# Kernel optimization log

Hardware: AMD Instinct MI355X
Metric: run time of the kernel (lower is better)

The kernel has to match this reference:

```python
import jax, jax.numpy as jnp
import numpy as np

N_NODES = 50000
LN_EPS = 1e-5


def setup_inputs() -> dict:
    key = jax.random.key(0)
    ks = jax.random.split(key, 8)
    d = 128
    E = 800000
    x = jax.random.normal(ks[0], (N_NODES, d), dtype=jnp.float32)
    edge_index = jax.random.randint(ks[1], (2, E), 0, N_NODES, dtype=jnp.int64)
    edge_weight = jax.random.uniform(ks[2], (E,), dtype=jnp.float32)
    s = 1.0 / np.sqrt(d)
    W1 = jax.random.normal(ks[3], (d, d), dtype=jnp.float32) * s
    W2 = jax.random.normal(ks[4], (d, d), dtype=jnp.float32) * s
    return {
        'x': x, 'edge_index': edge_index, 'edge_weight': edge_weight,
        'W1': W1, 'b1': jnp.zeros((d,), jnp.float32),
        'W2': W2, 'b2': jnp.zeros((d,), jnp.float32),
        'g1': jnp.ones((d,), jnp.float32), 'be1': jnp.zeros((d,), jnp.float32),
        'g2': jnp.ones((d,), jnp.float32), 'be2': jnp.zeros((d,), jnp.float32),
    }


def _layer_norm(h, gamma, beta):
    mu = jnp.mean(h, axis=-1, keepdims=True)
    var = jnp.mean(jnp.square(h - mu), axis=-1, keepdims=True)
    return (h - mu) * jax.lax.rsqrt(var + LN_EPS) * gamma + beta


def _gcn_layer(h, W, b, src, dst, ew):
    # GCNConv(add_self_loops=False, normalize=False): linear then edge scatter-add
    h = h @ W                                    # [N, d]
    msg = h[src] * ew[:, None]                   # [E, d] gather + weight
    agg = jax.ops.segment_sum(msg, dst, num_segments=N_NODES)  # scatter-add at target
    return agg + b


def reference(x, edge_index, edge_weight, W1, b1, W2, b2, g1, be1, g2, be2):
    src, dst = edge_index[0], edge_index[1]  # PyG: messages flow source -> target
    h = _gcn_layer(x, W1, b1, src, dst, edge_weight)
    h = jax.nn.relu(_layer_norm(h, g1, be1))  # dropout = identity (eval)
    h = _gcn_layer(h, W2, b2, src, dst, edge_weight)
    h = jax.nn.relu(_layer_norm(h, g2, be2))
    return h
```

## Files before the change

### kernel.cpp

```cpp
#include <hip/hip_runtime.h>
#include <hip/hip_fp16.h>
#include <stdint.h>

#define LN_EPS 1e-5f
#define G1 256
#define P1CAP 4096
#define P3CAP 6144
#define CAPB 6144

typedef __attribute__((ext_vector_type(8))) short s16x8;
typedef __attribute__((ext_vector_type(4))) float f32x4;

__device__ __forceinline__ float b2f(unsigned short u) {
    union { unsigned int i; float f; } v; v.i = ((unsigned int)u) << 16; return v.f;
}
__device__ __forceinline__ unsigned short f2b(float f) {
    union { float f; unsigned int i; } v; v.f = f;
    unsigned int u = v.i;
    return (unsigned short)((u + 0x7fffu + ((u >> 16) & 1u)) >> 16);
}
__device__ __forceinline__ unsigned int pk2(float a, float b) {
    return (unsigned int)f2b(a) | ((unsigned int)f2b(b) << 16);
}
__device__ __forceinline__ __half2 u2h2(unsigned int u) {
    union { unsigned int i; __half2 h; } v; v.i = u; return v.h;
}

__device__ __forceinline__ float rdf(const void* p, int i, int f32flag) {
    return f32flag ? ((const float*)p)[i] : b2f(((const unsigned short*)p)[i]);
}

__global__ void k_prep(const void* W1, const void* W2,
                       const void* b1, const void* b2,
                       const void* g1, const void* g2,
                       const void* be1, const void* be2,
                       unsigned short* __restrict__ Wt1, unsigned short* __restrict__ Wt2,
                       float* __restrict__ sm, const int* __restrict__ flags) {
    int t = threadIdx.x;
    int f = flags[0];
    int i = blockIdx.x * 256 + t;
    int k = i >> 7, j = i & 127;
    Wt1[j * 128 + k] = f2b(rdf(W1, i, f));
    Wt2[j * 128 + k] = f2b(rdf(W2, i, f));
    if (blockIdx.x == 0 && t < 128) {
        sm[t]       = rdf(b1, t, f);
        sm[128 + t] = rdf(b2, t, f);
        sm[256 + t] = rdf(g1, t, f);
        sm[384 + t] = rdf(g2, t, f);
        sm[512 + t] = rdf(be1, t, f);
        sm[640 + t] = rdf(be2, t, f);
    }
}

__global__ __launch_bounds__(256) void k_p1(const unsigned short* __restrict__ xu,
                                            const int* __restrict__ ei, const void* __restrict__ ew,
                                            int E, int B, int chunk,
                                            unsigned int* __restrict__ gA,
                                            unsigned char* __restrict__ g8,
                                            int* __restrict__ cnt2d, int* __restrict__ lofs2d,
                                            int* __restrict__ flags) {
    __shared__ int hist[256], cur[256], tmp[256];
    __shared__ unsigned int bin32[P1CAP];
    __shared__ unsigned char bin8[P1CAP];
    int t = threadIdx.x, g = blockIdx.x;
    if (t < 2) hist[t] = 0;
    __syncthreads();
    int c1 = 0;
    for (int i = t; i < 2048; i += 256)
        if (fabsf(b2f(xu[i])) > 1e6f) ++c1;
    if (c1) atomicAdd(&hist[0], c1);
    int mn = (E < 1024) ? E : 1024;
    int z = 0;
    for (int i = t; i < mn; i += 256)
        if (ei[2 * i + 1] == 0) ++z;
    if (z) atomicAdd(&hist[1], z);
    __syncthreads();
    int f32f = (hist[0] > 32) ? 1 : 0;
    int f64  = (hist[1] > (mn >> 1)) ? 1 : 0;
    if (g == 0 && t == 0) { flags[0] = f32f; flags[1] = f64; }
    __syncthreads();
    int base = g * chunk;
    int cnt = E - base; if (cnt > chunk) cnt = chunk; if (cnt < 0) cnt = 0;
    hist[t] = 0;
    __syncthreads();
    for (int i = t; i < cnt; i += 256) {
        int e = base + i;
        int d = f64 ? ei[2 * E + 2 * e] : ei[E + e];
        atomicAdd(&hist[d >> 8], 1);
    }
    __syncthreads();
    int v = hist[t];
    tmp[t] = v;
    __syncthreads();
    for (int d = 1; d < 256; d <<= 1) {
        int x = (t >= d) ? tmp[t - d] : 0;
        __syncthreads();
        tmp[t] += x;
        __syncthreads();
    }
    int excl = tmp[t] - v;
    cur[t] = excl;
    if (t < B) { cnt2d[t * G1 + g] = v; lofs2d[t * G1 + g] = excl; }
    __syncthreads();
    for (int i = t; i < cnt; i += 256) {
        int e = base + i;
        int d, sN;
        if (f64) { d = ei[2 * E + 2 * e]; sN = ei[2 * e]; }
        else     { d = ei[E + e];         sN = ei[e]; }
        float w = f32f ? ((const float*)ew)[e] : b2f(((const unsigned short*)ew)[e]);
        __half wh = __float2half(w);
        int p = atomicAdd(&cur[d >> 8], 1);
        bin32[p] = (unsigned int)(sN & 0xffff) | ((unsigned int)__half_as_ushort(wh) << 16);
        bin8[p]  = (unsigned char)(d & 255);
    }
    __syncthreads();
    for (int j = t; j < cnt; j += 256) {
        gA[base + j] = bin32[j];
        g8[base + j] = bin8[j];
    }
}

__global__ __launch_bounds__(256) void k_p3(const unsigned int* __restrict__ gA,
                                            const unsigned char* __restrict__ g8,
                                            const int* __restrict__ cnt2d,
                                            const int* __restrict__ lofs2d,
                                            unsigned int* __restrict__ edata,
                                            uint2* __restrict__ nfo,
                                            int N, int B, int chunk) {
    __shared__ unsigned int raw[P3CAP];
    __shared__ unsigned int srt[CAPB];
    __shared__ unsigned char r8[P3CAP];
    __shared__ int h[256], tmp[256];
    __shared__ int s_cnt;
    int b = blockIdx.x, t = threadIdx.x;
    int segc = cnt2d[b * G1 + t];
    int sbase = t * chunk + lofs2d[b * G1 + t];
    int v = segc;
    tmp[t] = v;
    __syncthreads();
    for (int d = 1; d < 256; d <<= 1) {
        int x = (t >= d) ? tmp[t - d] : 0;
        __syncthreads();
        tmp[t] += x;
        __syncthreads();
    }
    int lo = tmp[t] - v;
    if (t == 255) s_cnt = tmp[255];
    int j = 0;
    for (; j + 3 < segc; j += 4) {
        unsigned int a0 = gA[sbase + j], a1 = gA[sbase + j + 1];
        unsigned int a2 = gA[sbase + j + 2], a3 = gA[sbase + j + 3];
        unsigned char c0 = g8[sbase + j], c1 = g8[sbase + j + 1];
        unsigned char c2 = g8[sbase + j + 2], c3 = g8[sbase + j + 3];
        int i0 = lo + j;
        if (i0 + 3 < P3CAP) {
            raw[i0] = a0; raw[i0 + 1] = a1; raw[i0 + 2] = a2; raw[i0 + 3] = a3;
            r8[i0] = c0; r8[i0 + 1] = c1; r8[i0 + 2] = c2; r8[i0 + 3] = c3;
        }
    }
    for (; j < segc; ++j) {
        int idx = lo + j;
        if (idx < P3CAP) { raw[idx] = gA[sbase + j]; r8[idx] = g8[sbase + j]; }
    }
    h[t] = 0;
    __syncthreads();
    int cnt = s_cnt; if (cnt > P3CAP) cnt = P3CAP;
    for (int i = t; i < cnt; i += 256) atomicAdd(&h[r8[i]], 1);
    __syncthreads();
    int deg = h[t];
    int pd = (deg + 7) & ~7;
    tmp[t] = pd;
    __syncthreads();
    for (int d = 1; d < 256; d <<= 1) {
        int x = (t >= d) ? tmp[t - d] : 0;
        __syncthreads();
        tmp[t] += x;
        __syncthreads();
    }
    int pexcl = tmp[t] - pd;
    int padTot = tmp[255]; if (padTot > CAPB) padTot = CAPB;
    int node0 = b << 8;
    int gbase = b * CAPB;
    if (node0 + t < N) nfo[node0 + t] = make_uint2((unsigned)(gbase + pexcl), (unsigned)deg);
    h[t] = pexcl;
    for (int i = t; i < padTot; i += 256) srt[i] = 0;
    __syncthreads();
    for (int i = t; i < cnt; i += 256) {
        int p = atomicAdd(&h[r8[i]], 1);
        if (p < CAPB) srt[p] = raw[i];
    }
    __syncthreads();
    for (int i = t; i < padTot; i += 256) edata[gbase + i] = srt[i];
}

__global__ __launch_bounds__(256) void k_gemm(const void* __restrict__ X,
                                              const unsigned short* __restrict__ Wt,
                                              unsigned short* __restrict__ Hh, int N,
                                              const int* __restrict__ flags, int layer1) {
    __shared__ unsigned char lds[49152];
    unsigned char* xs = lds;
    unsigned char* wt = lds + 16384;
    int t = threadIdx.x;
    int node0 = blockIdx.x * 64;
    int f32in = layer1 ? flags[0] : 0;

#pragma unroll
    for (int it = 0; it < 8; ++it) {
        int c = t + it * 256;
        int row = c >> 4, cc = c & 15;
        uint4 v = *(const uint4*)(Wt + row * 128 + cc * 8);
        int off = (row * 256 + cc * 16) ^ ((row & 7) << 4);
        *(uint4*)(wt + off) = v;
    }
#pragma unroll
    for (int it = 0; it < 4; ++it) {
        int c = t + it * 256;
        int row = c >> 4, cc = c & 15;
        int g = node0 + row;
        uint4 v = make_uint4(0, 0, 0, 0);
        if (g < N) {
            if (f32in) {
                const float* xr = (const float*)X + (size_t)g * 128 + cc * 8;
                float4 f0 = *(const float4*)xr;
                float4 f1 = *(const float4*)(xr + 4);
                v.x = pk2(f0.x, f0.y); v.y = pk2(f0.z, f0.w);
                v.z = pk2(f1.x, f1.y); v.w = pk2(f1.z, f1.w);
            } else {
                v = *(const uint4*)((const unsigned short*)X + (size_t)g * 128 + cc * 8);
            }
        }
        int off = (row * 256 + cc * 16) ^ ((row & 7) << 4);
        *(uint4*)(xs + off) = v;
    }
    __syncthreads();

    int w = t >> 6, l = t & 63;
    int arow = l & 15;
    int apart = l >> 4;
    f32x4 acc[8];
#pragma unroll
    for (int ct = 0; ct < 8; ++ct) acc[ct] = (f32x4){0.f, 0.f, 0.f, 0.f};

#pragma unroll
    for (int ks = 0; ks < 4; ++ks) {
        int grow = w * 16 + arow;
        int aoff = (grow * 256 + ks * 64 + apart * 16) ^ ((grow & 7) << 4);
        s16x8 afrag = *(const s16x8*)(xs + aoff);
#pragma unroll
        for (int ct = 0; ct < 8; ++ct) {
            int brow = ct * 16 + arow;
            int boff = (brow * 256 + ks * 64 + apart * 16) ^ ((brow & 7) << 4);
            s16x8 bfrag = *(const s16x8*)(wt + boff);
            acc[ct] = __builtin_amdgcn_mfma_f32_16x16x32_bf16(afrag, bfrag, acc[ct], 0, 0, 0);
        }
    }
    int orow0 = node0 + w * 16 + apart * 4;
    int ocol = arow;
#pragma unroll
    for (int ct = 0; ct < 8; ++ct) {
#pragma unroll
        for (int r = 0; r < 4; ++r) {
            int g = orow0 + r;
            if (g < N) {
                __half hh = __float2half(acc[ct][r]);
                Hh[(size_t)g * 128 + ct * 16 + ocol] = __half_as_ushort(hh);
            }
        }
    }
}

template <bool FINAL>
__global__ __launch_bounds__(256) void k_agg_ln(const unsigned short* __restrict__ Hh,
                                                const unsigned int* __restrict__ edata,
                                                const uint2* __restrict__ nfo,
                                                const float* __restrict__ bias,
                                                const float* __restrict__ g,
                                                const float* __restrict__ be,
                                                unsigned short* __restrict__ outb,
                                                void* __restrict__ outAny,
                                                const int* __restrict__ flags, int N) {
    int t = threadIdx.x;
    int l16 = t & 15;
    int node = blockIdx.x * 16 + (t >> 4);
    if (node >= N) return;
    uint2 info = nfo[node];
    int base = (int)info.x, deg = (int)info.y;
    __half2 a01 = u2h2(0u), a23 = u2h2(0u), a45 = u2h2(0u), a67 = u2h2(0u);
    const uint4* Hl = (const uint4*)Hh + l16;
    for (int b0 = 0; b0 < deg; b0 += 8) {
        const uint4* ep = (const uint4*)(edata + base + b0);
        uint4 q0 = ep[0], q1 = ep[1];
        uint4 h0 = Hl[(size_t)(q0.x & 0xffffu) << 4];
        uint4 h1 = Hl[(size_t)(q0.y & 0xffffu) << 4];
        uint4 h2 = Hl[(size_t)(q0.z & 0xffffu) << 4];
        uint4 h3 = Hl[(size_t)(q0.w & 0xffffu) << 4];
        uint4 h4 = Hl[(size_t)(q1.x & 0xffffu) << 4];
        uint4 h5 = Hl[(size_t)(q1.y & 0xffffu) << 4];
        uint4 h6 = Hl[(size_t)(q1.z & 0xffffu) << 4];
        uint4 h7 = Hl[(size_t)(q1.w & 0xffffu) << 4];
        unsigned int wb; __half2 w2;
#define ACC8(hh, wsrc)                                                        \
        wb = (wsrc) >> 16; w2 = u2h2(wb | (wb << 16));                        \
        a01 = __hfma2(u2h2(hh.x), w2, a01); a23 = __hfma2(u2h2(hh.y), w2, a23); \
        a45 = __hfma2(u2h2(hh.z), w2, a45); a67 = __hfma2(u2h2(hh.w), w2, a67);
        ACC8(h0, q0.x) ACC8(h1, q0.y) ACC8(h2, q0.z) ACC8(h3, q0.w)
        ACC8(h4, q1.x) ACC8(h5, q1.y) ACC8(h6, q1.z) ACC8(h7, q1.w)
#undef ACC8
    }
    float4 bv0 = ((const float4*)bias)[2 * l16];
    float4 bv1 = ((const float4*)bias)[2 * l16 + 1];
    float a0 = __low2float(a01) + bv0.x, a1 = __high2float(a01) + bv0.y;
    float a2 = __low2float(a23) + bv0.z, a3 = __high2float(a23) + bv0.w;
    float a4 = __low2float(a45) + bv1.x, a5 = __high2float(a45) + bv1.y;
    float a6 = __low2float(a67) + bv1.z, a7 = __high2float(a67) + bv1.w;
    float s = ((a0 + a1) + (a2 + a3)) + ((a4 + a5) + (a6 + a7));
#pragma unroll
    for (int m = 8; m >= 1; m >>= 1) s += __shfl_xor(s, m, 64);
    float mu = s * (1.f / 128.f);
    float d0 = a0 - mu, d1 = a1 - mu, d2 = a2 - mu, d3 = a3 - mu;
    float d4 = a4 - mu, d5 = a5 - mu, d6 = a6 - mu, d7 = a7 - mu;
    float q = ((d0 * d0 + d1 * d1) + (d2 * d2 + d3 * d3)) +
              ((d4 * d4 + d5 * d5) + (d6 * d6 + d7 * d7));
#pragma unroll
    for (int m = 8; m >= 1; m >>= 1) q += __shfl_xor(q, m, 64);
    float rs = rsqrtf(q * (1.f / 128.f) + LN_EPS);
    float4 gv0 = ((const float4*)g)[2 * l16], gv1 = ((const float4*)g)[2 * l16 + 1];
    float4 bev0 = ((const float4*)be)[2 * l16], bev1 = ((const float4*)be)[2 * l16 + 1];
    float r0 = fmaxf(d0 * rs * gv0.x + bev0.x, 0.f);
    float r1 = fmaxf(d1 * rs * gv0.y + bev0.y, 0.f);
    float r2 = fmaxf(d2 * rs * gv0.z + bev0.z, 0.f);
    float r3 = fmaxf(d3 * rs * gv0.w + bev0.w, 0.f);
    float r4 = fmaxf(d4 * rs * gv1.x + bev1.x, 0.f);
    float r5 = fmaxf(d5 * rs * gv1.y + bev1.y, 0.f);
    float r6 = fmaxf(d6 * rs * gv1.z + bev1.z, 0.f);
    float r7 = fmaxf(d7 * rs * gv1.w + bev1.w, 0.f);
    if (FINAL) {
        if (flags[0]) {
            float4* o = (float4*)outAny + (size_t)node * 32 + 2 * l16;
            o[0] = make_float4(r0, r1, r2, r3);
            o[1] = make_float4(r4, r5, r6, r7);
        } else {
            uint4 o;
            o.x = pk2(r0, r1); o.y = pk2(r2, r3);
            o.z = pk2(r4, r5); o.w = pk2(r6, r7);
            ((uint4*)outAny)[(size_t)node * 16 + l16] = o;
        }
    } else {
        uint4 o;
        o.x = pk2(r0, r1); o.y = pk2(r2, r3);
        o.z = pk2(r4, r5); o.w = pk2(r6, r7);
        ((uint4*)outb)[(size_t)node * 16 + l16] = o;
    }
}

extern "C" void kernel_launch(void* const* d_in, const int* in_sizes, int n_in,
                              void* d_out, int out_size, void* d_ws, size_t ws_size,
                              hipStream_t stream) {
    const unsigned short* x_u16 = (const unsigned short*)d_in[0];
    const int*            ei    = (const int*)d_in[1];

    const int N = in_sizes[0] / 128;
    const int E = in_sizes[2];
    const int B = (N + 255) >> 8;
    const int chunk = (E + G1 - 1) / G1;

    unsigned short* Xb = (unsigned short*)d_ws;
    unsigned short* Hh = Xb + (size_t)N * 128;
    unsigned int* gA    = (unsigned int*)(Hh + (size_t)N * 128);
    unsigned int* edata = gA + E;
    unsigned char* g8   = (unsigned char*)(edata + (size_t)B * CAPB);
    int* cnt2d  = (int*)(g8 + ((E + 3) & ~3));
    int* lofs2d = cnt2d + 65536;
    uint2* nfo  = (uint2*)(lofs2d + 65536);
    int* flags  = (int*)(nfo + N);
    unsigned short* Wt1 = (unsigned short*)(flags + 8);
    unsigned short* Wt2 = Wt1 + 16384;
    float* sm   = (float*)(Wt2 + 16384);
    float* b1f  = sm;
    float* b2f_ = sm + 128;
    float* g1f  = sm + 256;
    float* g2f  = sm + 384;
    float* be1f = sm + 512;
    float* be2f = sm + 640;

    const int nodeBlocks = (N + 15) / 16;
    const int gemmBlocks = (N + 63) / 64;

    k_p1<<<G1, 256, 0, stream>>>(x_u16, ei, d_in[2], E, B, chunk, gA, g8, cnt2d, lofs2d, flags);
    k_prep<<<64, 256, 0, stream>>>(d_in[3], d_in[5], d_in[4], d_in[6],
                                   d_in[7], d_in[9], d_in[8], d_in[10],
                                   Wt1, Wt2, sm, flags);
    k_p3<<<B, 256, 0, stream>>>(gA, g8, cnt2d, lofs2d, edata, nfo, N, B, chunk);

    k_gemm<<<gemmBlocks, 256, 0, stream>>>(d_in[0], Wt1, Hh, N, flags, 1);
    k_agg_ln<false><<<nodeBlocks, 256, 0, stream>>>(Hh, edata, nfo, b1f, g1f, be1f, Xb, nullptr, flags, N);

    k_gemm<<<gemmBlocks, 256, 0, stream>>>(Xb, Wt2, Hh, N, flags, 0);
    k_agg_ln<true><<<nodeBlocks, 256, 0, stream>>>(Hh, edata, nfo, b2f_, g2f, be2f, nullptr, d_out, flags, N);
}
```

Measured before the change: 121.7 us.

## Fuse GCN pipeline into one cooperative persistent kernel with grid syncs

```diff
diff --git a/kernel.cpp b/kernel.cpp
--- a/kernel.cpp
+++ b/kernel.cpp
@@ -1,11 +1,13 @@
 #include <hip/hip_runtime.h>
 #include <hip/hip_fp16.h>
+#include <hip/hip_cooperative_groups.h>
 #include <stdint.h>
+
+namespace cg = cooperative_groups;
 
 #define LN_EPS 1e-5f
 #define G1 256
-#define P1CAP 4096
-#define P3CAP 6144
+#define P3CAP 5632
 #define CAPB 6144
 
 typedef __attribute__((ext_vector_type(8))) short s16x8;
@@ -25,67 +27,65 @@
 __device__ __forceinline__ __half2 u2h2(unsigned int u) {
     union { unsigned int i; __half2 h; } v; v.i = u; return v.h;
 }
-
 __device__ __forceinline__ float rdf(const void* p, int i, int f32flag) {
     return f32flag ? ((const float*)p)[i] : b2f(((const unsigned short*)p)[i]);
 }
 
-__global__ void k_prep(const void* W1, const void* W2,
-                       const void* b1, const void* b2,
-                       const void* g1, const void* g2,
-                       const void* be1, const void* be2,
-                       unsigned short* __restrict__ Wt1, unsigned short* __restrict__ Wt2,
-                       float* __restrict__ sm, const int* __restrict__ flags) {
-    int t = threadIdx.x;
-    int f = flags[0];
-    int i = blockIdx.x * 256 + t;
-    int k = i >> 7, j = i & 127;
-    Wt1[j * 128 + k] = f2b(rdf(W1, i, f));
-    Wt2[j * 128 + k] = f2b(rdf(W2, i, f));
-    if (blockIdx.x == 0 && t < 128) {
-        sm[t]       = rdf(b1, t, f);
-        sm[128 + t] = rdf(b2, t, f);
-        sm[256 + t] = rdf(g1, t, f);
-        sm[384 + t] = rdf(g2, t, f);
-        sm[512 + t] = rdf(be1, t, f);
-        sm[640 + t] = rdf(be2, t, f);
-    }
-}
-
-__global__ __launch_bounds__(256) void k_p1(const unsigned short* __restrict__ xu,
-                                            const int* __restrict__ ei, const void* __restrict__ ew,
-                                            int E, int B, int chunk,
-                                            unsigned int* __restrict__ gA,
-                                            unsigned char* __restrict__ g8,
-                                            int* __restrict__ cnt2d, int* __restrict__ lofs2d,
-                                            int* __restrict__ flags) {
-    __shared__ int hist[256], cur[256], tmp[256];
-    __shared__ unsigned int bin32[P1CAP];
-    __shared__ unsigned char bin8[P1CAP];
-    int t = threadIdx.x, g = blockIdx.x;
-    if (t < 2) hist[t] = 0;
+struct Params {
+    const unsigned short* xu;
+    const int* ei;
+    const void* ew;
+    const void* W1; const void* W2;
+    const void* b1; const void* b2;
+    const void* g1; const void* g2;
+    const void* be1; const void* be2;
+    unsigned short* Wt1; unsigned short* Wt2;
+    float* sm;
+    unsigned int* gA;
+    unsigned char* g8;
+    int* cnt2d; int* lofs2d;
+    unsigned int* edata;
+    uint2* nfo;
+    unsigned short* Hh;
+    unsigned short* Hh2;
+    void* out;
+    int N, E, B, chunk, nodeBlocks, gemmBlocks;
+};
+
+__device__ __forceinline__ void detect_types(const Params& p, int t, int* scratch,
+                                             int& f32f, int& f64) {
+    if (t < 2) scratch[t] = 0;
     __syncthreads();
     int c1 = 0;
     for (int i = t; i < 2048; i += 256)
-        if (fabsf(b2f(xu[i])) > 1e6f) ++c1;
-    if (c1) atomicAdd(&hist[0], c1);
-    int mn = (E < 1024) ? E : 1024;
+        if (fabsf(b2f(p.xu[i])) > 1e6f) ++c1;
+    if (c1) atomicAdd(&scratch[0], c1);
+    int mn = (p.E < 1024) ? p.E : 1024;
     int z = 0;
     for (int i = t; i < mn; i += 256)
-        if (ei[2 * i + 1] == 0) ++z;
-    if (z) atomicAdd(&hist[1], z);
-    __syncthreads();
-    int f32f = (hist[0] > 32) ? 1 : 0;
-    int f64  = (hist[1] > (mn >> 1)) ? 1 : 0;
-    if (g == 0 && t == 0) { flags[0] = f32f; flags[1] = f64; }
-    __syncthreads();
-    int base = g * chunk;
-    int cnt = E - base; if (cnt > chunk) cnt = chunk; if (cnt < 0) cnt = 0;
+        if (p.ei[2 * i + 1] == 0) ++z;
+    if (z) atomicAdd(&scratch[1], z);
+    __syncthreads();
+    f32f = (scratch[0] > 32) ? 1 : 0;
+    f64  = (scratch[1] > (mn >> 1)) ? 1 : 0;
+    __syncthreads();
+}
+
+__device__ __forceinline__ void phaseA_bin(const Params& p, int vb, int t,
+                                           unsigned char* lds, int f32f, int f64) {
+    int* hist = (int*)lds;
+    int* cur  = (int*)(lds + 1024);
+    int* tmp  = (int*)(lds + 2048);
+    unsigned int* bin32 = (unsigned int*)(lds + 3072);
+    unsigned char* bin8 = lds + 19456;
+    const int E = p.E, B = p.B;
+    int base = vb * p.chunk;
+    int cnt = E - base; if (cnt > p.chunk) cnt = p.chunk; if (cnt < 0) cnt = 0;
     hist[t] = 0;
     __syncthreads();
     for (int i = t; i < cnt; i += 256) {
         int e = base + i;
-        int d = f64 ? ei[2 * E + 2 * e] : ei[E + e];
+        int d = f64 ? p.ei[2 * E + 2 * e] : p.ei[E + e];
         atomicAdd(&hist[d >> 8], 1);
     }
     __syncthreads();
@@ -100,41 +100,53 @@
     }
     int excl = tmp[t] - v;
     cur[t] = excl;
-    if (t < B) { cnt2d[t * G1 + g] = v; lofs2d[t * G1 + g] = excl; }
+    if (t < B) { p.cnt2d[t * G1 + vb] = v; p.lofs2d[t * G1 + vb] = excl; }
     __syncthreads();
     for (int i = t; i < cnt; i += 256) {
         int e = base + i;
         int d, sN;
-        if (f64) { d = ei[2 * E + 2 * e]; sN = ei[2 * e]; }
-        else     { d = ei[E + e];         sN = ei[e]; }
-        float w = f32f ? ((const float*)ew)[e] : b2f(((const unsigned short*)ew)[e]);
+        if (f64) { d = p.ei[2 * E + 2 * e]; sN = p.ei[2 * e]; }
+        else     { d = p.ei[E + e];         sN = p.ei[e]; }
+        float w = f32f ? ((const float*)p.ew)[e] : b2f(((const unsigned short*)p.ew)[e]);
         __half wh = __float2half(w);
-        int p = atomicAdd(&cur[d >> 8], 1);
-        bin32[p] = (unsigned int)(sN & 0xffff) | ((unsigned int)__half_as_ushort(wh) << 16);
-        bin8[p]  = (unsigned char)(d & 255);
+        int pos = atomicAdd(&cur[d >> 8], 1);
+        bin32[pos] = (unsigned int)(sN & 0xffff) | ((unsigned int)__half_as_ushort(wh) << 16);
+        bin8[pos]  = (unsigned char)(d & 255);
     }
     __syncthreads();
     for (int j = t; j < cnt; j += 256) {
-        gA[base + j] = bin32[j];
-        g8[base + j] = bin8[j];
-    }
-}
-
-__global__ __launch_bounds__(256) void k_p3(const unsigned int* __restrict__ gA,
-                                            const unsigned char* __restrict__ g8,
-                                            const int* __restrict__ cnt2d,
-                                            const int* __restrict__ lofs2d,
-                                            unsigned int* __restrict__ edata,
-                                            uint2* __restrict__ nfo,
-                                            int N, int B, int chunk) {
-    __shared__ unsigned int raw[P3CAP];
-    __shared__ unsigned int srt[CAPB];
-    __shared__ unsigned char r8[P3CAP];
-    __shared__ int h[256], tmp[256];
-    __shared__ int s_cnt;
-    int b = blockIdx.x, t = threadIdx.x;
-    int segc = cnt2d[b * G1 + t];
-    int sbase = t * chunk + lofs2d[b * G1 + t];
+        p.gA[base + j] = bin32[j];
+        p.g8[base + j] = bin8[j];
+    }
+    __syncthreads();
+}
+
+__device__ __forceinline__ void phaseA_prep(const Params& p, int vb, int t, int f32f) {
+    int i = (vb - G1) * 256 + t;
+    int k = i >> 7, j = i & 127;
+    p.Wt1[j * 128 + k] = f2b(rdf(p.W1, i, f32f));
+    p.Wt2[j * 128 + k] = f2b(rdf(p.W2, i, f32f));
+    if (vb == G1 && t < 128) {
+        p.sm[t]       = rdf(p.b1, t, f32f);
+        p.sm[128 + t] = rdf(p.b2, t, f32f);
+        p.sm[256 + t] = rdf(p.g1, t, f32f);
+        p.sm[384 + t] = rdf(p.g2, t, f32f);
+        p.sm[512 + t] = rdf(p.be1, t, f32f);
+        p.sm[640 + t] = rdf(p.be2, t, f32f);
+    }
+}
+
+__device__ __forceinline__ void phaseB_p3(const Params& p, int vb, int t,
+                                          unsigned char* lds) {
+    unsigned int* raw = (unsigned int*)lds;
+    unsigned char* r8 = lds + 22528;
+    int* h    = (int*)(lds + 28160);
+    int* tmp  = (int*)(lds + 29184);
+    int* scnt = (int*)(lds + 30208);
+    const int N = p.N;
+    int b = vb;
+    int segc = p.cnt2d[b * G1 + t];
+    int sbase = t * p.chunk + p.lofs2d[b * G1 + t];
     int v = segc;
     tmp[t] = v;
     __syncthreads();
@@ -145,13 +157,13 @@
         __syncthreads();
     }
     int lo = tmp[t] - v;
-    if (t == 255) s_cnt = tmp[255];
+    if (t == 255) scnt[0] = tmp[255];
     int j = 0;
     for (; j + 3 < segc; j += 4) {
-        unsigned int a0 = gA[sbase + j], a1 = gA[sbase + j + 1];
-        unsigned int a2 = gA[sbase + j + 2], a3 = gA[sbase + j + 3];
-        unsigned char c0 = g8[sbase + j], c1 = g8[sbase + j + 1];
-        unsigned char c2 = g8[sbase + j + 2], c3 = g8[sbase + j + 3];
+        unsigned int a0 = p.gA[sbase + j], a1 = p.gA[sbase + j + 1];
+        unsigned int a2 = p.gA[sbase + j + 2], a3 = p.gA[sbase + j + 3];
+        unsigned char c0 = p.g8[sbase + j], c1 = p.g8[sbase + j + 1];
+        unsigned char c2 = p.g8[sbase + j + 2], c3 = p.g8[sbase + j + 3];
         int i0 = lo + j;
         if (i0 + 3 < P3CAP) {
             raw[i0] = a0; raw[i0 + 1] = a1; raw[i0 + 2] = a2; raw[i0 + 3] = a3;
@@ -160,11 +172,11 @@
     }
     for (; j < segc; ++j) {
         int idx = lo + j;
-        if (idx < P3CAP) { raw[idx] = gA[sbase + j]; r8[idx] = g8[sbase + j]; }
+        if (idx < P3CAP) { raw[idx] = p.gA[sbase + j]; r8[idx] = p.g8[sbase + j]; }
     }
     h[t] = 0;
     __syncthreads();
-    int cnt = s_cnt; if (cnt > P3CAP) cnt = P3CAP;
+    int cnt = scnt[0]; if (cnt > P3CAP) cnt = P3CAP;
     for (int i = t; i < cnt; i += 256) atomicAdd(&h[r8[i]], 1);
     __syncthreads();
     int deg = h[t];
@@ -181,66 +193,49 @@
     int padTot = tmp[255]; if (padTot > CAPB) padTot = CAPB;
     int node0 = b << 8;
     int gbase = b * CAPB;
-    if (node0 + t < N) nfo[node0 + t] = make_uint2((unsigned)(gbase + pexcl), (unsigned)deg);
+    if (node0 + t < N) p.nfo[node0 + t] = make_uint2((unsigned)(gbase + pexcl), (unsigned)deg);
     h[t] = pexcl;
-    for (int i = t; i < padTot; i += 256) srt[i] = 0;
+    for (int i = t; i < padTot; i += 256) p.edata[gbase + i] = 0;
     __syncthreads();
     for (int i = t; i < cnt; i += 256) {
-        int p = atomicAdd(&h[r8[i]], 1);
-        if (p < CAPB) srt[p] = raw[i];
-    }
-    __syncthreads();
-    for (int i = t; i < padTot; i += 256) edata[gbase + i] = srt[i];
-}
-
-__global__ __launch_bounds__(256) void k_gemm(const void* __restrict__ X,
-                                              const unsigned short* __restrict__ Wt,
-                                              unsigned short* __restrict__ Hh, int N,
-                                              const int* __restrict__ flags, int layer1) {
-    __shared__ unsigned char lds[49152];
+        int pos = atomicAdd(&h[r8[i]], 1);
+        if (pos < CAPB) p.edata[gbase + pos] = raw[i];
+    }
+    __syncthreads();
+}
+
+__device__ __forceinline__ void phaseB_gemm1(const Params& p, int vb, int t,
+                                             unsigned char* lds, int f32f) {
     unsigned char* xs = lds;
-    unsigned char* wt = lds + 16384;
-    int t = threadIdx.x;
-    int node0 = blockIdx.x * 64;
-    int f32in = layer1 ? flags[0] : 0;
-
-#pragma unroll
-    for (int it = 0; it < 8; ++it) {
-        int c = t + it * 256;
-        int row = c >> 4, cc = c & 15;
-        uint4 v = *(const uint4*)(Wt + row * 128 + cc * 8);
-        int off = (row * 256 + cc * 16) ^ ((row & 7) << 4);
-        *(uint4*)(wt + off) = v;
-    }
+    const int N = p.N;
+    int node0 = (vb - p.B) * 64;
 #pragma unroll
     for (int it = 0; it < 4; ++it) {
         int c = t + it * 256;
         int row = c >> 4, cc = c & 15;
-        int g = node0 + row;
+        int gg = node0 + row;
         uint4 v = make_uint4(0, 0, 0, 0);
-        if (g < N) {
-            if (f32in) {
-                const float* xr = (const float*)X + (size_t)g * 128 + cc * 8;
+        if (gg < N) {
+            if (f32f) {
+                const float* xr = (const float*)p.xu + (size_t)gg * 128 + cc * 8;
                 float4 f0 = *(const float4*)xr;
                 float4 f1 = *(const float4*)(xr + 4);
                 v.x = pk2(f0.x, f0.y); v.y = pk2(f0.z, f0.w);
                 v.z = pk2(f1.x, f1.y); v.w = pk2(f1.z, f1.w);
             } else {
-                v = *(const uint4*)((const unsigned short*)X + (size_t)g * 128 + cc * 8);
+                v = *(const uint4*)((const unsigned short*)p.xu + (size_t)gg * 128 + cc * 8);
             }
         }
         int off = (row * 256 + cc * 16) ^ ((row & 7) << 4);
         *(uint4*)(xs + off) = v;
     }
     __syncthreads();
-
     int w = t >> 6, l = t & 63;
     int arow = l & 15;
     int apart = l >> 4;
     f32x4 acc[8];
 #pragma unroll
     for (int ct = 0; ct < 8; ++ct) acc[ct] = (f32x4){0.f, 0.f, 0.f, 0.f};
-
 #pragma unroll
     for (int ks = 0; ks < 4; ++ks) {
         int grow = w * 16 + arow;
@@ -248,45 +243,36 @@
         s16x8 afrag = *(const s16x8*)(xs + aoff);
 #pragma unroll
         for (int ct = 0; ct < 8; ++ct) {
-            int brow = ct * 16 + arow;
-            int boff = (brow * 256 + ks * 64 + apart * 16) ^ ((brow & 7) << 4);
-            s16x8 bfrag = *(const s16x8*)(wt + boff);
+            s16x8 bfrag = *(const s16x8*)(p.Wt1 + (ct * 16 + arow) * 128 + ks * 32 + apart * 8);
             acc[ct] = __builtin_amdgcn_mfma_f32_16x16x32_bf16(afrag, bfrag, acc[ct], 0, 0, 0);
         }
     }
     int orow0 = node0 + w * 16 + apart * 4;
-    int ocol = arow;
 #pragma unroll
     for (int ct = 0; ct < 8; ++ct) {
 #pragma unroll
         for (int r = 0; r < 4; ++r) {
-            int g = orow0 + r;
-            if (g < N) {
+            int gg = orow0 + r;
+            if (gg < N) {
                 __half hh = __float2half(acc[ct][r]);
-                Hh[(size_t)g * 128 + ct * 16 + ocol] = __half_as_ushort(hh);
+                p.Hh[(size_t)gg * 128 + ct * 16 + arow] = __half_as_ushort(hh);
             }
         }
     }
-}
-
-template <bool FINAL>
-__global__ __launch_bounds__(256) void k_agg_ln(const unsigned short* __restrict__ Hh,
-                                                const unsigned int* __restrict__ edata,
-                                                const uint2* __restrict__ nfo,
-                                                const float* __restrict__ bias,
-                                                const float* __restrict__ g,
-                                                const float* __restrict__ be,
-                                                unsigned short* __restrict__ outb,
-                                                void* __restrict__ outAny,
-                                                const int* __restrict__ flags, int N) {
-    int t = threadIdx.x;
-    int l16 = t & 15;
-    int node = blockIdx.x * 16 + (t >> 4);
-    if (node >= N) return;
+    __syncthreads();
+}
+
+__device__ __forceinline__ uint4 agg_ln_row(const unsigned short* __restrict__ Hs,
+                                            const unsigned int* __restrict__ edata,
+                                            const uint2* __restrict__ nfo,
+                                            const float* __restrict__ bias,
+                                            const float* __restrict__ gam,
+                                            const float* __restrict__ bet,
+                                            int node, int l16, float* r) {
     uint2 info = nfo[node];
     int base = (int)info.x, deg = (int)info.y;
     __half2 a01 = u2h2(0u), a23 = u2h2(0u), a45 = u2h2(0u), a67 = u2h2(0u);
-    const uint4* Hl = (const uint4*)Hh + l16;
+    const uint4* Hl = (const uint4*)Hs + l16;
     for (int b0 = 0; b0 < deg; b0 += 8) {
         const uint4* ep = (const uint4*)(edata + base + b0);
         uint4 q0 = ep[0], q1 = ep[1];
@@ -324,77 +310,201 @@
 #pragma unroll
     for (int m = 8; m >= 1; m >>= 1) q += __shfl_xor(q, m, 64);
     float rs = rsqrtf(q * (1.f / 128.f) + LN_EPS);
-    float4 gv0 = ((const float4*)g)[2 * l16], gv1 = ((const float4*)g)[2 * l16 + 1];
-    float4 bev0 = ((const float4*)be)[2 * l16], bev1 = ((const float4*)be)[2 * l16 + 1];
-    float r0 = fmaxf(d0 * rs * gv0.x + bev0.x, 0.f);
-    float r1 = fmaxf(d1 * rs * gv0.y + bev0.y, 0.f);
-    float r2 = fmaxf(d2 * rs * gv0.z + bev0.z, 0.f);
-    float r3 = fmaxf(d3 * rs * gv0.w + bev0.w, 0.f);
-    float r4 = fmaxf(d4 * rs * gv1.x + bev1.x, 0.f);
-    float r5 = fmaxf(d5 * rs * gv1.y + bev1.y, 0.f);
-    float r6 = fmaxf(d6 * rs * gv1.z + bev1.z, 0.f);
-    float r7 = fmaxf(d7 * rs * gv1.w + bev1.w, 0.f);
-    if (FINAL) {
-        if (flags[0]) {
-            float4* o = (float4*)outAny + (size_t)node * 32 + 2 * l16;
-            o[0] = make_float4(r0, r1, r2, r3);
-            o[1] = make_float4(r4, r5, r6, r7);
-        } else {
-            uint4 o;
-            o.x = pk2(r0, r1); o.y = pk2(r2, r3);
-            o.z = pk2(r4, r5); o.w = pk2(r6, r7);
-            ((uint4*)outAny)[(size_t)node * 16 + l16] = o;
+    float4 gv0 = ((const float4*)gam)[2 * l16], gv1 = ((const float4*)gam)[2 * l16 + 1];
+    float4 bev0 = ((const float4*)bet)[2 * l16], bev1 = ((const float4*)bet)[2 * l16 + 1];
+    r[0] = fmaxf(d0 * rs * gv0.x + bev0.x, 0.f);
+    r[1] = fmaxf(d1 * rs * gv0.y + bev0.y, 0.f);
+    r[2] = fmaxf(d2 * rs * gv0.z + bev0.z, 0.f);
+    r[3] = fmaxf(d3 * rs * gv0.w + bev0.w, 0.f);
+    r[4] = fmaxf(d4 * rs * gv1.x + bev1.x, 0.f);
+    r[5] = fmaxf(d5 * rs * gv1.y + bev1.y, 0.f);
+    r[6] = fmaxf(d6 * rs * gv1.z + bev1.z, 0.f);
+    r[7] = fmaxf(d7 * rs * gv1.w + bev1.w, 0.f);
+    uint4 o;
+    o.x = pk2(r[0], r[1]); o.y = pk2(r[2], r[3]);
+    o.z = pk2(r[4], r[5]); o.w = pk2(r[6], r[7]);
+    return o;
+}
+
+__device__ __forceinline__ void phaseC(const Params& p, int vb, int t,
+                                       unsigned char* lds) {
+    unsigned char* xs = lds;
+    const float* b1f  = p.sm;
+    const float* g1f  = p.sm + 256;
+    const float* be1f = p.sm + 512;
+    const int N = p.N;
+    int l16 = t & 15;
+    int nodeLocal = t >> 4;
+    int node0 = vb * 16;
+    int node = node0 + nodeLocal;
+    uint4 xv = make_uint4(0, 0, 0, 0);
+    float rr[8];
+    if (node < N)
+        xv = agg_ln_row(p.Hh, p.edata, p.nfo, b1f, g1f, be1f, node, l16, rr);
+    __syncthreads();
+    {
+        int off = (nodeLocal * 256 + l16 * 16) ^ ((nodeLocal & 7) << 4);
+        *(uint4*)(xs + off) = xv;
+    }
+    __syncthreads();
+    int w = t >> 6, l = t & 63;
+    int arow = l & 15;
+    int apart = l >> 4;
+    f32x4 acc0 = (f32x4){0.f, 0.f, 0.f, 0.f};
+    f32x4 acc1 = (f32x4){0.f, 0.f, 0.f, 0.f};
+#pragma unroll
+    for (int ks = 0; ks < 4; ++ks) {
+        int aoff = (arow * 256 + ks * 64 + apart * 16) ^ ((arow & 7) << 4);
+        s16x8 afrag = *(const s16x8*)(xs + aoff);
+        s16x8 bf0 = *(const s16x8*)(p.Wt2 + ((w * 2 + 0) * 16 + arow) * 128 + ks * 32 + apart * 8);
+        s16x8 bf1 = *(const s16x8*)(p.Wt2 + ((w * 2 + 1) * 16 + arow) * 128 + ks * 32 + apart * 8);
+        acc0 = __builtin_amdgcn_mfma_f32_16x16x32_bf16(afrag, bf0, acc0, 0, 0, 0);
+        acc1 = __builtin_amdgcn_mfma_f32_16x16x32_bf16(afrag, bf1, acc1, 0, 0, 0);
+    }
+    int orow0 = node0 + apart * 4;
+#pragma unroll
+    for (int r = 0; r < 4; ++r) {
+        int gg = orow0 + r;
+        if (gg < N) {
+            __half h0 = __float2half(acc0[r]);
+            __half h1 = __float2half(acc1[r]);
+            p.Hh2[(size_t)gg * 128 + (w * 2 + 0) * 16 + arow] = __half_as_ushort(h0);
+            p.Hh2[(size_t)gg * 128 + (w * 2 + 1) * 16 + arow] = __half_as_ushort(h1);
         }
+    }
+}
+
+__device__ __forceinline__ void phaseD(const Params& p, int vb, int t, int f32f) {
+    const float* b2f_ = p.sm + 128;
+    const float* g2f  = p.sm + 384;
+    const float* be2f = p.sm + 640;
+    int l16 = t & 15;
+    int node = vb * 16 + (t >> 4);
+    if (node >= p.N) return;
+    float rr[8];
+    uint4 o = agg_ln_row(p.Hh2, p.edata, p.nfo, b2f_, g2f, be2f, node, l16, rr);
+    if (f32f) {
+        float4* op = (float4*)p.out + (size_t)node * 32 + 2 * l16;
+        op[0] = make_float4(rr[0], rr[1], rr[2], rr[3]);
+        op[1] = make_float4(rr[4], rr[5], rr[6], rr[7]);
     } else {
-        uint4 o;
-        o.x = pk2(r0, r1); o.y = pk2(r2, r3);
-        o.z = pk2(r4, r5); o.w = pk2(r6, r7);
-        ((uint4*)outb)[(size_t)node * 16 + l16] = o;
-    }
+        ((uint4*)p.out)[(size_t)node * 16 + l16] = o;
+    }
+}
+
+__global__ __launch_bounds__(256, 4) void k_fused(Params p) {
+    cg::grid_group grid = cg::this_grid();
+    __shared__ __align__(16) unsigned char lds[30720];
+    int t = threadIdx.x;
+    int f32f, f64;
+    detect_types(p, t, (int*)lds, f32f, f64);
+
+    for (int vb = blockIdx.x; vb < G1 + 64; vb += gridDim.x) {
+        if (vb >= G1) phaseA_prep(p, vb, t, f32f);
+        else          phaseA_bin(p, vb, t, lds, f32f, f64);
+    }
+    grid.sync();
+    for (int vb = blockIdx.x; vb < p.B + p.gemmBlocks; vb += gridDim.x) {
+        if (vb < p.B) phaseB_p3(p, vb, t, lds);
+        else          phaseB_gemm1(p, vb, t, lds, f32f);
+    }
+    grid.sync();
+    for (int vb = blockIdx.x; vb < p.nodeBlocks; vb += gridDim.x)
+        phaseC(p, vb, t, lds);
+    grid.sync();
+    for (int vb = blockIdx.x; vb < p.nodeBlocks; vb += gridDim.x)
+        phaseD(p, vb, t, f32f);
+}
+
+__global__ __launch_bounds__(256) void k_fA(Params p) {
+    __shared__ __align__(16) unsigned char lds[23552];
+    int t = threadIdx.x, vb = blockIdx.x;
+    int f32f, f64;
+    detect_types(p, t, (int*)lds, f32f, f64);
+    if (vb >= G1) phaseA_prep(p, vb, t, f32f);
+    else          phaseA_bin(p, vb, t, lds, f32f, f64);
+}
+__global__ __launch_bounds__(256) void k_fB(Params p) {
+    __shared__ __align__(16) unsigned char lds[30720];
+    int t = threadIdx.x, vb = blockIdx.x;
+    int f32f, f64;
+    detect_types(p, t, (int*)lds, f32f, f64);
+    if (vb < p.B) phaseB_p3(p, vb, t, lds);
+    else          phaseB_gemm1(p, vb, t, lds, f32f);
+}
+__global__ __launch_bounds__(256) void k_fC(Params p) {
+    __shared__ __align__(16) unsigned char lds[4096];
+    int t = threadIdx.x;
+    phaseC(p, blockIdx.x, t, lds);
+}
+__global__ __launch_bounds__(256) void k_fD(Params p) {
+    __shared__ __align__(16) unsigned char lds[64];
+    int t = threadIdx.x;
+    int f32f, f64;
+    detect_types(p, t, (int*)lds, f32f, f64);
+    phaseD(p, blockIdx.x, t, f32f);
 }
 
 extern "C" void kernel_launch(void* const* d_in, const int* in_sizes, int n_in,
                               void* d_out, int out_size, void* d_ws, size_t ws_size,
                               hipStream_t stream) {
-    const unsigned short* x_u16 = (const unsigned short*)d_in[0];
-    const int*            ei    = (const int*)d_in[1];
-
     const int N = in_sizes[0] / 128;
     const int E = in_sizes[2];
     const int B = (N + 255) >> 8;
     const int chunk = (E + G1 - 1) / G1;
 
-    unsigned short* Xb = (unsigned short*)d_ws;
-    unsigned short* Hh = Xb + (size_t)N * 128;
+    unsigned short* Hh2 = (unsigned short*)d_ws;
+    unsigned short* Hh  = Hh2 + (size_t)N * 128;
     unsigned int* gA    = (unsigned int*)(Hh + (size_t)N * 128);
     unsigned int* edata = gA + E;
     unsigned char* g8   = (unsigned char*)(edata + (size_t)B * CAPB);
     int* cnt2d  = (int*)(g8 + ((E + 3) & ~3));
     int* lofs2d = cnt2d + 65536;
     uint2* nfo  = (uint2*)(lofs2d + 65536);
-    int* flags  = (int*)(nfo + N);
-    unsigned short* Wt1 = (unsigned short*)(flags + 8);
+    unsigned short* Wt1 = (unsigned short*)(nfo + N);
     unsigned short* Wt2 = Wt1 + 16384;
     float* sm   = (float*)(Wt2 + 16384);
-    float* b1f  = sm;
-    float* b2f_ = sm + 128;
-    float* g1f  = sm + 256;
-    float* g2f  = sm + 384;
-    float* be1f = sm + 512;
-    float* be2f = sm + 640;
-
-    const int nodeBlocks = (N + 15) / 16;
-    const int gemmBlocks = (N + 63) / 64;
-
-    k_p1<<<G1, 256, 0, stream>>>(x_u16, ei, d_in[2], E, B, chunk, gA, g8, cnt2d, lofs2d, flags);
-    k_prep<<<64, 256, 0, stream>>>(d_in[3], d_in[5], d_in[4], d_in[6],
-                                   d_in[7], d_in[9], d_in[8], d_in[10],
-                                   Wt1, Wt2, sm, flags);
-    k_p3<<<B, 256, 0, stream>>>(gA, g8, cnt2d, lofs2d, edata, nfo, N, B, chunk);
-
-    k_gemm<<<gemmBlocks, 256, 0, stream>>>(d_in[0], Wt1, Hh, N, flags, 1);
-    k_agg_ln<false><<<nodeBlocks, 256, 0, stream>>>(Hh, edata, nfo, b1f, g1f, be1f, Xb, nullptr, flags, N);
-
-    k_gemm<<<gemmBlocks, 256, 0, stream>>>(Xb, Wt2, Hh, N, flags, 0);
-    k_agg_ln<true><<<nodeBlocks, 256, 0, stream>>>(Hh, edata, nfo, b2f_, g2f, be2f, nullptr, d_out, flags, N);
-}
+
+    Params prm;
+    prm.xu = (const unsigned short*)d_in[0];
+    prm.ei = (const int*)d_in[1];
+    prm.ew = d_in[2];
+    prm.W1 = d_in[3]; prm.W2 = d_in[5];
+    prm.b1 = d_in[4]; prm.b2 = d_in[6];
+    prm.g1 = d_in[7]; prm.g2 = d_in[9];
+    prm.be1 = d_in[8]; prm.be2 = d_in[10];
+    prm.Wt1 = Wt1; prm.Wt2 = Wt2; prm.sm = sm;
+    prm.gA = gA; prm.g8 = g8;
+    prm.cnt2d = cnt2d; prm.lofs2d = lofs2d;
+    prm.edata = edata; prm.nfo = nfo;
+    prm.Hh = Hh; prm.Hh2 = Hh2;
+    prm.out = d_out;
+    prm.N = N; prm.E = E; prm.B = B; prm.chunk = chunk;
+    prm.nodeBlocks = (N + 15) / 16;
+    prm.gemmBlocks = (N + 63) / 64;
+
+    bool launched = false;
+    int coop = 0, dev = 0;
+    hipGetDevice(&dev);
+    hipDeviceGetAttribute(&coop, hipDeviceAttributeCooperativeLaunch, dev);
+    if (coop) {
+        int numCU = 0;
+        hipDeviceGetAttribute(&numCU, hipDeviceAttributeMultiprocessorCount, dev);
+        int occ = 0;
+        hipError_t oe = hipOccupancyMaxActiveBlocksPerMultiprocessor(&occ, k_fused, 256, 0);
+        if (oe == hipSuccess && occ > 0 && numCU > 0) {
+            int grid = occ * numCU;
+            if (grid > 2048) grid = 2048;
+            void* args[] = { &prm };
+            hipError_t le = hipLaunchCooperativeKernel((void*)k_fused, dim3(grid),
+                                                       dim3(256), args, 0, stream);
+            launched = (le == hipSuccess);
+        }
+    }
+    if (!launched) {
+        k_fA<<<G1 + 64, 256, 0, stream>>>(prm);
+        k_fB<<<B + prm.gemmBlocks, 256, 0, stream>>>(prm);
+        k_fC<<<prm.nodeBlocks, 256, 0, stream>>>(prm);
+        k_fD<<<prm.nodeBlocks, 256, 0, stream>>>(prm);
+    }
+}
```

After: 325.3 us. 167% more time.
